# Kernel tuning notes

Hardware: AMD Instinct MI355X
Metric: run time of the kernel (lower is better)

The kernel has to match this reference:

```python
import jax, jax.numpy as jnp
import numpy as np

B, T, L, D = 512, 100, 256, 128
DEPTH = 8                 # perfect binary tree depth -> path length DEPTH+1
P = DEPTH + 1
N_PER_TREE = 2 * L - 1    # 511 nodes per tree (heap layout)
N_TOTAL = T * N_PER_TREE  # 51100 global nodes


def _build_paths():
    # Heap layout per tree: internal nodes 0..L-2, leaves L-1..2L-2.
    # Path for leaf l = chain of heap ancestors from root to leaf.
    local = np.zeros((L, P), dtype=np.int32)
    for l in range(L):
        node = L - 1 + l
        chain = []
        while True:
            chain.append(node)
            if node == 0:
                break
            node = (node - 1) // 2
        local[l] = np.array(chain[::-1], dtype=np.int32)
    offs = (np.arange(T, dtype=np.int32) * N_PER_TREE)[:, None, None]
    return local[None, :, :] + offs  # [T, L, P] global node ids


def setup_inputs() -> dict:
    key = jax.random.key(0)
    k1, k2, k3, k4, k5, k6 = jax.random.split(key, 6)
    paths = jnp.asarray(_build_paths())
    # GBDT multi-hot: exactly one activated leaf per tree per sample
    leaf = jax.random.randint(k1, (B, T), 0, L)
    cross = (jnp.zeros((B, T, L), jnp.float32)
             .at[jnp.arange(B)[:, None], jnp.arange(T)[None, :], leaf]
             .set(1.0)
             .reshape(B, T * L))
    s = 1.0 / float(np.sqrt(D))  # torch LSTM init range
    node_emb = jax.random.normal(k2, (N_TOTAL, D), jnp.float32) * 0.01
    w_ih = jax.random.uniform(k3, (4 * D, D), jnp.float32, -s, s)
    w_hh = jax.random.uniform(k4, (4 * D, D), jnp.float32, -s, s)
    b_ih = jax.random.uniform(k5, (4 * D,), jnp.float32, -s, s)
    b_hh = jax.random.uniform(k6, (4 * D,), jnp.float32, -s, s)
    return {"cross_features": cross, "node_emb": node_emb, "w_ih": w_ih,
            "w_hh": w_hh, "b_ih": b_ih, "b_hh": b_hh, "paths": paths}


def _lstm_last_h(x, w_ih, w_hh, b_ih, b_hh):
    # x: [S, P, D] -> final hidden state [S, D]; torch gate order i, f, g, o
    S = x.shape[0]
    d = w_hh.shape[1]
    bias = b_ih + b_hh

    def step(carry, x_t):
        h, c = carry
        g = x_t @ w_ih.T + h @ w_hh.T + bias          # [S, 4D]
        i, f, gg, o = jnp.split(g, 4, axis=-1)
        c = jax.nn.sigmoid(f) * c + jax.nn.sigmoid(i) * jnp.tanh(gg)
        h = jax.nn.sigmoid(o) * jnp.tanh(c)
        return (h, c), None

    h0 = jnp.zeros((S, d), x.dtype)
    (h, _), _ = jax.lax.scan(step, (h0, h0), jnp.swapaxes(x, 0, 1))
    return h


def reference(cross_features, node_emb, w_ih, w_hh, b_ih, b_hh, paths):
    t, l, p = paths.shape
    b = cross_features.shape[0]
    d = node_emb.shape[1]
    cf = cross_features.reshape(b, t, l)
    leaf = jnp.argmax(cf, axis=-1)                    # [B, T] activated leaf per tree
    active = jnp.any(cf > 0, axis=-1)                 # [B, T] tree has an activated leaf
    node_ids = paths[jnp.arange(t)[None, :], leaf]    # [B, T, P] root-to-leaf global ids
    x = node_emb[node_ids].reshape(b * t, p, d)       # batched path gather
    h = _lstm_last_h(x, w_ih, w_hh, b_ih, b_hh).reshape(b, t, d)
    return jnp.where(active[..., None], h, jnp.zeros((), h.dtype))
```

## Files before the change

### kernel.cpp

```cpp
#include <hip/hip_runtime.h>
#include <math.h>


#define B_N 512
#define T_N 100
#define L_N 256
#define D_N 128
#define NPT 511

typedef __attribute__((ext_vector_type(8))) short short8;
typedef __attribute__((ext_vector_type(4))) float f32x4;
typedef __attribute__((ext_vector_type(4))) unsigned short ushort4v;

__device__ __forceinline__ unsigned short f2bf(float f) {
    unsigned u = __float_as_uint(f);
    return (unsigned short)((u + 0x7FFFu + ((u >> 16) & 1u)) >> 16);
}
__device__ __forceinline__ float bf2f(unsigned short b) {
    return __uint_as_float(((unsigned)b) << 16);
}
__device__ __forceinline__ float fsigmoid(float x) {
    return __builtin_amdgcn_rcpf(1.f + __builtin_amdgcn_exp2f(-1.44269504f * x));
}
__device__ __forceinline__ float ftanh(float x) {
    return 1.f - 2.f * __builtin_amdgcn_rcpf(1.f + __builtin_amdgcn_exp2f(2.88539009f * x));
}
__device__ __forceinline__ void keepreg(short8 &x) {
    asm volatile("" : "+v"(x));
}

__global__ __launch_bounds__(256) void pack_kernel(const float* __restrict__ w_ih,
                                                   const float* __restrict__ w_hh,
                                                   const float* __restrict__ b_ih,
                                                   const float* __restrict__ b_hh,
                                                   unsigned short* __restrict__ Bhi,
                                                   unsigned short* __restrict__ Blo,
                                                   float* __restrict__ bias) {
    const int idx = blockIdx.x * 256 + threadIdx.x;
    const int k  = idx & 255;
    const int np = idx >> 8;
    const float val = (k < 128) ? w_ih[(size_t)np * 128 + k]
                                : w_hh[(size_t)np * 128 + (k - 128)];
    const unsigned short hi = f2bf(val);
    const int kb = k >> 5, krel = k & 31, quad = krel >> 3, e = krel & 7;
    const int tn = np >> 4, col = np & 15, lane = quad * 16 + col;
    Bhi[(((size_t)kb * 32 + tn) * 64 + lane) * 8 + e] = hi;
    if (kb >= 4) {
        const unsigned short lo = f2bf(val - bf2f(hi));
        Blo[((((size_t)kb - 4) * 32 + tn) * 64 + lane) * 8 + e] = lo;
    }
    if (k == 0) bias[np] = b_ih[np] + b_hh[np];
}

__global__ __launch_bounds__(512, 2) void tree_kernel(
    const float* __restrict__ node_emb,
    const unsigned short* __restrict__ Bhi,
    const unsigned short* __restrict__ Blo,
    const float* __restrict__ bias,
    float* __restrict__ h8)
{
    __shared__ float hbuf[2][2][16][132];
    __shared__ float cbuf[2][2][16][132];
    __shared__ float h7buf[2][32][132];
    __shared__ unsigned short AhiF[8 * 4 * 512];
    __shared__ unsigned short AloF[4 * 4 * 512];

    const int tp   = blockIdx.x >> 2;
    const int s    = blockIdx.x & 3;
    const int t0   = tp * 2;
    const int tid  = threadIdx.x;
    const int widx = tid >> 6;
    const int lane = tid & 63;
    const int ml   = lane & 15;
    const int quad = lane >> 4;
    const int j    = widx * 16 + ml;

    const float bi = bias[j];
    const float bf = bias[128 + j];
    const float bg = bias[256 + j];
    const float bo = bias[384 + j];

    const short8* Bh8 = reinterpret_cast<const short8*>(Bhi);
    const short8* Bl8 = reinterpret_cast<const short8*>(Blo);
    const short8* Ah8 = reinterpret_cast<const short8*>(AhiF);
    const short8* Al8 = reinterpret_cast<const short8*>(AloF);

    short8 bhR[8][4], blR[4][4];
    #pragma unroll
    for (int kb = 0; kb < 8; ++kb)
        #pragma unroll
        for (int g = 0; g < 4; ++g)
            bhR[kb][g] = Bh8[(kb * 32 + g * 8 + widx) * 64 + lane];
    #pragma unroll
    for (int kb = 0; kb < 4; ++kb)
        #pragma unroll
        for (int g = 0; g < 4; ++g)
            blR[kb][g] = Bl8[(kb * 32 + g * 8 + widx) * 64 + lane];
    #pragma unroll
    for (int kb = 0; kb < 8; ++kb)
        #pragma unroll
        for (int g = 0; g < 4; ++g)
            keepreg(bhR[kb][g]);
    #pragma unroll
    for (int kb = 0; kb < 4; ++kb)
        #pragma unroll
        for (int g = 0; g < 4; ++g)
            keepreg(blR[kb][g]);

    for (int d = 0; d <= 6; ++d) {
        const int Mrows = (d == 0) ? 1 : (d == 1) ? 2 : (1 << (d - 2));
        const int pbase = (d >= 2) ? (s << (d - 2)) : 0;
        const bool root = (d == 0);
        const int cur = d & 1, prv = cur ^ 1;

        #pragma unroll
        for (int h2 = 0; h2 < 4; ++h2) {
            const int r5 = tid & 31;
            const int u  = r5 >> 4, r = r5 & 15;
            const int k4 = (tid >> 5) + h2 * 16;
            const int k  = k4 * 4;
            int p = r; if (p > Mrows - 1) p = Mrows - 1;
            float4 v;
            if (k < 128) {
                const int local = (1 << d) - 1 + pbase + p;
                v = *reinterpret_cast<const float4*>(
                        node_emb + (size_t)((t0 + u) * NPT + local) * D_N + k);
            } else if (root) {
                v = make_float4(0.f, 0.f, 0.f, 0.f);
            } else {
                const int pr = (d == 2) ? (s >> 1) : (p >> 1);
                v = *reinterpret_cast<const float4*>(&hbuf[prv][u][pr][k - 128]);
            }
            const int kb = k >> 5, qk = (k & 31) >> 3, e0 = k & 4;
            const ushort4v hv = { f2bf(v.x), f2bf(v.y), f2bf(v.z), f2bf(v.w) };
            *reinterpret_cast<ushort4v*>(
                &AhiF[((kb * 4 + u) * 64 + qk * 16 + r) * 8 + e0]) = hv;
            if (k >= 128) {
                const ushort4v lv = { f2bf(v.x - bf2f(hv.x)), f2bf(v.y - bf2f(hv.y)),
                                      f2bf(v.z - bf2f(hv.z)), f2bf(v.w - bf2f(hv.w)) };
                *reinterpret_cast<ushort4v*>(
                    &AloF[(((kb - 4) * 4 + u) * 64 + qk * 16 + r) * 8 + e0]) = lv;
            }
        }
        __syncthreads();

        #pragma unroll
        for (int u = 0; u < 2; ++u) {
            float cpre[4];
            #pragma unroll
            for (int rr = 0; rr < 4; ++rr) {
                int m = quad * 4 + rr;
                if (m > Mrows - 1) m = Mrows - 1;
                const int pr = (d == 2) ? (s >> 1) : (m >> 1);
                cpre[rr] = root ? 0.f : cbuf[prv][u][pr][j];
            }

            f32x4 acc[4];
            #pragma unroll
            for (int g = 0; g < 4; ++g) acc[g] = (f32x4)0.f;

            #pragma unroll
            for (int kb = 0; kb < 8; ++kb) {
                const short8 ah = Ah8[(kb * 4 + u) * 64 + lane];
                short8 al;
                if (kb >= 4) al = Al8[((kb - 4) * 4 + u) * 64 + lane];
                #pragma unroll
                for (int g = 0; g < 4; ++g) {
                    acc[g] = __builtin_amdgcn_mfma_f32_16x16x32_bf16(
                        ah, bhR[kb][g], acc[g], 0, 0, 0);
                    if (kb >= 4) {
                        acc[g] = __builtin_amdgcn_mfma_f32_16x16x32_bf16(
                            ah, blR[kb - 4][g], acc[g], 0, 0, 0);
                        acc[g] = __builtin_amdgcn_mfma_f32_16x16x32_bf16(
                            al, bhR[kb][g], acc[g], 0, 0, 0);
                    }
                }
            }

            #pragma unroll
            for (int rr = 0; rr < 4; ++rr) {
                const int m = quad * 4 + rr;
                if (m < Mrows) {
                    const float ig = fsigmoid(acc[0][rr] + bi);
                    const float fg = fsigmoid(acc[1][rr] + bf);
                    const float gv = ftanh(acc[2][rr] + bg);
                    const float og = fsigmoid(acc[3][rr] + bo);
                    const float cn = fg * cpre[rr] + ig * gv;
                    const float hn = og * ftanh(cn);
                    hbuf[cur][u][m][j] = hn;
                    cbuf[cur][u][m][j] = cn;
                }
            }
        }
        __syncthreads();
    }

    {
        #pragma unroll
        for (int h2 = 0; h2 < 8; ++h2) {
            const int r6 = tid & 63;
            const int u  = r6 >> 5, m = r6 & 31;
            const int k4 = (tid >> 6) + h2 * 8;
            const int k  = k4 * 4;
            const int mt = r6 >> 4, mlr = r6 & 15;
            float4 v;
            if (k < 128) {
                const int local = 127 + s * 32 + m;
                v = *reinterpret_cast<const float4*>(
                        node_emb + (size_t)((t0 + u) * NPT + local) * D_N + k);
            } else {
                v = *reinterpret_cast<const float4*>(&hbuf[0][u][m >> 1][k - 128]);
            }
            const int kb = k >> 5, qk = (k & 31) >> 3, e0 = k & 4;
            const ushort4v hv = { f2bf(v.x), f2bf(v.y), f2bf(v.z), f2bf(v.w) };
            *reinterpret_cast<ushort4v*>(
                &AhiF[((kb * 4 + mt) * 64 + qk * 16 + mlr) * 8 + e0]) = hv;
            if (k >= 128) {
                const ushort4v lv = { f2bf(v.x - bf2f(hv.x)), f2bf(v.y - bf2f(hv.y)),
                                      f2bf(v.z - bf2f(hv.z)), f2bf(v.w - bf2f(hv.w)) };
                *reinterpret_cast<ushort4v*>(
                    &AloF[(((kb - 4) * 4 + mt) * 64 + qk * 16 + mlr) * 8 + e0]) = lv;
            }
        }
        __syncthreads();

        float cpreA[4][4];
        #pragma unroll
        for (int mt = 0; mt < 4; ++mt) {
            const int u = mt >> 1;
            #pragma unroll
            for (int rr = 0; rr < 4; ++rr) {
                const int m = (mt & 1) * 16 + quad * 4 + rr;
                cpreA[mt][rr] = cbuf[0][u][m >> 1][j];
            }
        }
        __syncthreads();

        #pragma unroll
        for (int mt = 0; mt < 4; ++mt) {
            const int u = mt >> 1;
            f32x4 acc[4];
            #pragma unroll
            for (int g = 0; g < 4; ++g) acc[g] = (f32x4)0.f;
            #pragma unroll
            for (int kb = 0; kb < 8; ++kb) {
                const short8 ah = Ah8[(kb * 4 + mt) * 64 + lane];
                short8 al;
                if (kb >= 4) al = Al8[((kb - 4) * 4 + mt) * 64 + lane];
                #pragma unroll
                for (int g = 0; g < 4; ++g) {
                    acc[g] = __builtin_amdgcn_mfma_f32_16x16x32_bf16(
                        ah, bhR[kb][g], acc[g], 0, 0, 0);
                    if (kb >= 4) {
                        acc[g] = __builtin_amdgcn_mfma_f32_16x16x32_bf16(
                            ah, blR[kb - 4][g], acc[g], 0, 0, 0);
                        acc[g] = __builtin_amdgcn_mfma_f32_16x16x32_bf16(
                            al, bhR[kb][g], acc[g], 0, 0, 0);
                    }
                }
            }
            #pragma unroll
            for (int rr = 0; rr < 4; ++rr) {
                const int m = (mt & 1) * 16 + quad * 4 + rr;
                const float ig = fsigmoid(acc[0][rr] + bi);
                const float fg = fsigmoid(acc[1][rr] + bf);
                const float gv = ftanh(acc[2][rr] + bg);
                const float og = fsigmoid(acc[3][rr] + bo);
                const float cn = fg * cpreA[mt][rr] + ig * gv;
                const float hn = og * ftanh(cn);
                h7buf[u][m][j] = hn;
                cbuf[m >> 4][u][m & 15][j] = cn;
            }
        }
        __syncthreads();
    }

    for (int pp = 0; pp < 2; ++pp) {
        #pragma unroll
        for (int h2 = 0; h2 < 8; ++h2) {
            const int r6   = tid & 63;
            const int u    = r6 >> 5, m31 = r6 & 31;
            const int mrow = pp * 32 + m31;
            const int k4   = (tid >> 6) + h2 * 8;
            const int k    = k4 * 4;
            const int mt   = r6 >> 4, mlr = r6 & 15;
            float4 v;
            if (k < 128) {
                const int local = 255 + s * 64 + mrow;
                v = *reinterpret_cast<const float4*>(
                        node_emb + (size_t)((t0 + u) * NPT + local) * D_N + k);
            } else {
                v = *reinterpret_cast<const float4*>(&h7buf[u][mrow >> 1][k - 128]);
            }
            const int kb = k >> 5, qk = (k & 31) >> 3, e0 = k & 4;
            const ushort4v hv = { f2bf(v.x), f2bf(v.y), f2bf(v.z), f2bf(v.w) };
            *reinterpret_cast<ushort4v*>(
                &AhiF[((kb * 4 + mt) * 64 + qk * 16 + mlr) * 8 + e0]) = hv;
            if (k >= 128) {
                const ushort4v lv = { f2bf(v.x - bf2f(hv.x)), f2bf(v.y - bf2f(hv.y)),
                                      f2bf(v.z - bf2f(hv.z)), f2bf(v.w - bf2f(hv.w)) };
                *reinterpret_cast<ushort4v*>(
                    &AloF[(((kb - 4) * 4 + mt) * 64 + qk * 16 + mlr) * 8 + e0]) = lv;
            }
        }
        __syncthreads();

        #pragma unroll
        for (int mt = 0; mt < 4; ++mt) {
            const int u = mt >> 1;
            float cpre[4];
            #pragma unroll
            for (int rr = 0; rr < 4; ++rr) {
                const int mrow = pp * 32 + (mt & 1) * 16 + quad * 4 + rr;
                const int c7r  = mrow >> 1;
                cpre[rr] = cbuf[c7r >> 4][u][c7r & 15][j];
            }
            f32x4 acc[4];
            #pragma unroll
            for (int g = 0; g < 4; ++g) acc[g] = (f32x4)0.f;
            #pragma unroll
            for (int kb = 0; kb < 8; ++kb) {
                const short8 ah = Ah8[(kb * 4 + mt) * 64 + lane];
                short8 al;
                if (kb >= 4) al = Al8[((kb - 4) * 4 + mt) * 64 + lane];
                #pragma unroll
                for (int g = 0; g < 4; ++g) {
                    acc[g] = __builtin_amdgcn_mfma_f32_16x16x32_bf16(
                        ah, bhR[kb][g], acc[g], 0, 0, 0);
                    if (kb >= 4) {
                        acc[g] = __builtin_amdgcn_mfma_f32_16x16x32_bf16(
                            ah, blR[kb - 4][g], acc[g], 0, 0, 0);
                        acc[g] = __builtin_amdgcn_mfma_f32_16x16x32_bf16(
                            al, bhR[kb][g], acc[g], 0, 0, 0);
                    }
                }
            }
            #pragma unroll
            for (int rr = 0; rr < 4; ++rr) {
                const int mrow = pp * 32 + (mt & 1) * 16 + quad * 4 + rr;
                const float ig = fsigmoid(acc[0][rr] + bi);
                const float fg = fsigmoid(acc[1][rr] + bf);
                const float gv = ftanh(acc[2][rr] + bg);
                const float og = fsigmoid(acc[3][rr] + bo);
                const float cn = fg * cpre[rr] + ig * gv;
                const float hn = og * ftanh(cn);
                h8[(size_t)(((t0 + u) << 8) + s * 64 + mrow) * D_N + j] = hn;
            }
        }
        __syncthreads();
    }
}

__global__ __launch_bounds__(256) void gather_kernel(const float* __restrict__ cross,
                                                     const float* __restrict__ h8,
                                                     float* __restrict__ out) {
    const int bt   = blockIdx.x * 4 + (threadIdx.x >> 6);
    const int lane = threadIdx.x & 63;
    const int t    = bt % T_N;
    const float4 v = reinterpret_cast<const float4*>(cross + (size_t)bt * L_N)[lane];
    int idx = -1;
    if      (v.x > 0.f) idx = lane * 4 + 0;
    else if (v.y > 0.f) idx = lane * 4 + 1;
    else if (v.z > 0.f) idx = lane * 4 + 2;
    else if (v.w > 0.f) idx = lane * 4 + 3;
    const unsigned long long m = __ballot(idx >= 0);
    int lf = -1;
    if (m != 0ULL) {
        const int first = __builtin_ctzll(m);
        lf = __shfl(idx, first);
    }
    float2 o = make_float2(0.f, 0.f);
    if (lf >= 0)
        o = reinterpret_cast<const float2*>(h8 + (size_t)(t * L_N + lf) * D_N)[lane];
    reinterpret_cast<float2*>(out + (size_t)bt * D_N)[lane] = o;
}

extern "C" void kernel_launch(void* const* d_in, const int* in_sizes, int n_in,
                              void* d_out, int out_size, void* d_ws, size_t ws_size,
                              hipStream_t stream) {
    const float* cross    = (const float*)d_in[0];
    const float* node_emb = (const float*)d_in[1];
    const float* w_ih     = (const float*)d_in[2];
    const float* w_hh     = (const float*)d_in[3];
    const float* b_ih     = (const float*)d_in[4];
    const float* b_hh     = (const float*)d_in[5];
    float* out = (float*)d_out;
    float* ws  = (float*)d_ws;

    float* h8   = ws;
    float* bias = h8 + (size_t)51200 * D_N;
    unsigned short* Bhi = (unsigned short*)(bias + 512);
    unsigned short* Blo = Bhi + 131072;

    pack_kernel<<<512, 256, 0, stream>>>(w_ih, w_hh, b_ih, b_hh, Bhi, Blo, bias);

    tree_kernel<<<(T_N / 2) * 4, 512, 0, stream>>>(node_emb, Bhi, Blo, bias, h8);

    gather_kernel<<<(B_N * T_N) / 4, 256, 0, stream>>>(cross, h8, out);
}
```

Before: 198.2 us.

## Stream LSTM weights from memory per k-block and reuse across row tiles

```diff
diff --git a/kernel.cpp b/kernel.cpp
--- a/kernel.cpp
+++ b/kernel.cpp
@@ -24,9 +24,6 @@
 }
 __device__ __forceinline__ float ftanh(float x) {
     return 1.f - 2.f * __builtin_amdgcn_rcpf(1.f + __builtin_amdgcn_exp2f(2.88539009f * x));
-}
-__device__ __forceinline__ void keepreg(short8 &x) {
-    asm volatile("" : "+v"(x));
 }
 
 __global__ __launch_bounds__(256) void pack_kernel(const float* __restrict__ w_ih,
@@ -85,28 +82,6 @@
     const short8* Ah8 = reinterpret_cast<const short8*>(AhiF);
     const short8* Al8 = reinterpret_cast<const short8*>(AloF);
 
-    short8 bhR[8][4], blR[4][4];
-    #pragma unroll
-    for (int kb = 0; kb < 8; ++kb)
-        #pragma unroll
-        for (int g = 0; g < 4; ++g)
-            bhR[kb][g] = Bh8[(kb * 32 + g * 8 + widx) * 64 + lane];
-    #pragma unroll
-    for (int kb = 0; kb < 4; ++kb)
-        #pragma unroll
-        for (int g = 0; g < 4; ++g)
-            blR[kb][g] = Bl8[(kb * 32 + g * 8 + widx) * 64 + lane];
-    #pragma unroll
-    for (int kb = 0; kb < 8; ++kb)
-        #pragma unroll
-        for (int g = 0; g < 4; ++g)
-            keepreg(bhR[kb][g]);
-    #pragma unroll
-    for (int kb = 0; kb < 4; ++kb)
-        #pragma unroll
-        for (int g = 0; g < 4; ++g)
-            keepreg(blR[kb][g]);
-
     for (int d = 0; d <= 6; ++d) {
         const int Mrows = (d == 0) ? 1 : (d == 1) ? 2 : (1 << (d - 2));
         const int pbase = (d >= 2) ? (s << (d - 2)) : 0;
@@ -144,48 +119,49 @@
         }
         __syncthreads();
 
+        f32x4 acc[2][4];
+        #pragma unroll
+        for (int u = 0; u < 2; ++u)
+            #pragma unroll
+            for (int g = 0; g < 4; ++g) acc[u][g] = (f32x4)0.f;
+
+        #pragma unroll
+        for (int kb = 0; kb < 8; ++kb) {
+            const short8 ah0 = Ah8[(kb * 4 + 0) * 64 + lane];
+            const short8 ah1 = Ah8[(kb * 4 + 1) * 64 + lane];
+            short8 al0, al1;
+            if (kb >= 4) {
+                al0 = Al8[((kb - 4) * 4 + 0) * 64 + lane];
+                al1 = Al8[((kb - 4) * 4 + 1) * 64 + lane];
+            }
+            #pragma unroll
+            for (int g = 0; g < 4; ++g) {
+                const short8 bh = Bh8[(kb * 32 + g * 8 + widx) * 64 + lane];
+                acc[0][g] = __builtin_amdgcn_mfma_f32_16x16x32_bf16(ah0, bh, acc[0][g], 0, 0, 0);
+                acc[1][g] = __builtin_amdgcn_mfma_f32_16x16x32_bf16(ah1, bh, acc[1][g], 0, 0, 0);
+                if (kb >= 4) {
+                    const short8 bl = Bl8[((kb - 4) * 32 + g * 8 + widx) * 64 + lane];
+                    acc[0][g] = __builtin_amdgcn_mfma_f32_16x16x32_bf16(ah0, bl, acc[0][g], 0, 0, 0);
+                    acc[1][g] = __builtin_amdgcn_mfma_f32_16x16x32_bf16(ah1, bl, acc[1][g], 0, 0, 0);
+                    acc[0][g] = __builtin_amdgcn_mfma_f32_16x16x32_bf16(al0, bh, acc[0][g], 0, 0, 0);
+                    acc[1][g] = __builtin_amdgcn_mfma_f32_16x16x32_bf16(al1, bh, acc[1][g], 0, 0, 0);
+                }
+            }
+        }
+
         #pragma unroll
         for (int u = 0; u < 2; ++u) {
-            float cpre[4];
-            #pragma unroll
-            for (int rr = 0; rr < 4; ++rr) {
-                int m = quad * 4 + rr;
-                if (m > Mrows - 1) m = Mrows - 1;
-                const int pr = (d == 2) ? (s >> 1) : (m >> 1);
-                cpre[rr] = root ? 0.f : cbuf[prv][u][pr][j];
-            }
-
-            f32x4 acc[4];
-            #pragma unroll
-            for (int g = 0; g < 4; ++g) acc[g] = (f32x4)0.f;
-
-            #pragma unroll
-            for (int kb = 0; kb < 8; ++kb) {
-                const short8 ah = Ah8[(kb * 4 + u) * 64 + lane];
-                short8 al;
-                if (kb >= 4) al = Al8[((kb - 4) * 4 + u) * 64 + lane];
-                #pragma unroll
-                for (int g = 0; g < 4; ++g) {
-                    acc[g] = __builtin_amdgcn_mfma_f32_16x16x32_bf16(
-                        ah, bhR[kb][g], acc[g], 0, 0, 0);
-                    if (kb >= 4) {
-                        acc[g] = __builtin_amdgcn_mfma_f32_16x16x32_bf16(
-                            ah, blR[kb - 4][g], acc[g], 0, 0, 0);
-                        acc[g] = __builtin_amdgcn_mfma_f32_16x16x32_bf16(
-                            al, bhR[kb][g], acc[g], 0, 0, 0);
-                    }
-                }
-            }
-
             #pragma unroll
             for (int rr = 0; rr < 4; ++rr) {
                 const int m = quad * 4 + rr;
                 if (m < Mrows) {
-                    const float ig = fsigmoid(acc[0][rr] + bi);
-                    const float fg = fsigmoid(acc[1][rr] + bf);
-                    const float gv = ftanh(acc[2][rr] + bg);
-                    const float og = fsigmoid(acc[3][rr] + bo);
-                    const float cn = fg * cpre[rr] + ig * gv;
+                    const int pr = (d == 2) ? (s >> 1) : (m >> 1);
+                    const float cp = root ? 0.f : cbuf[prv][u][pr][j];
+                    const float ig = fsigmoid(acc[u][0][rr] + bi);
+                    const float fg = fsigmoid(acc[u][1][rr] + bf);
+                    const float gv = ftanh(acc[u][2][rr] + bg);
+                    const float og = fsigmoid(acc[u][3][rr] + bo);
+                    const float cn = fg * cp + ig * gv;
                     const float hn = og * ftanh(cn);
                     hbuf[cur][u][m][j] = hn;
                     cbuf[cur][u][m][j] = cn;
@@ -224,52 +200,53 @@
         }
         __syncthreads();
 
-        float cpreA[4][4];
+        f32x4 acc[4][4];
+        #pragma unroll
+        for (int mt = 0; mt < 4; ++mt)
+            #pragma unroll
+            for (int g = 0; g < 4; ++g) acc[mt][g] = (f32x4)0.f;
+
+        #pragma unroll
+        for (int kb = 0; kb < 8; ++kb) {
+            short8 ah[4], al[4];
+            #pragma unroll
+            for (int mt = 0; mt < 4; ++mt) {
+                ah[mt] = Ah8[(kb * 4 + mt) * 64 + lane];
+                if (kb >= 4) al[mt] = Al8[((kb - 4) * 4 + mt) * 64 + lane];
+            }
+            #pragma unroll
+            for (int g = 0; g < 4; ++g) {
+                const short8 bh = Bh8[(kb * 32 + g * 8 + widx) * 64 + lane];
+                #pragma unroll
+                for (int mt = 0; mt < 4; ++mt)
+                    acc[mt][g] = __builtin_amdgcn_mfma_f32_16x16x32_bf16(ah[mt], bh, acc[mt][g], 0, 0, 0);
+                if (kb >= 4) {
+                    const short8 bl = Bl8[((kb - 4) * 32 + g * 8 + widx) * 64 + lane];
+                    #pragma unroll
+                    for (int mt = 0; mt < 4; ++mt) {
+                        acc[mt][g] = __builtin_amdgcn_mfma_f32_16x16x32_bf16(ah[mt], bl, acc[mt][g], 0, 0, 0);
+                        acc[mt][g] = __builtin_amdgcn_mfma_f32_16x16x32_bf16(al[mt], bh, acc[mt][g], 0, 0, 0);
+                    }
+                }
+            }
+        }
+
         #pragma unroll
         for (int mt = 0; mt < 4; ++mt) {
             const int u = mt >> 1;
             #pragma unroll
             for (int rr = 0; rr < 4; ++rr) {
                 const int m = (mt & 1) * 16 + quad * 4 + rr;
-                cpreA[mt][rr] = cbuf[0][u][m >> 1][j];
-            }
-        }
-        __syncthreads();
-
-        #pragma unroll
-        for (int mt = 0; mt < 4; ++mt) {
-            const int u = mt >> 1;
-            f32x4 acc[4];
-            #pragma unroll
-            for (int g = 0; g < 4; ++g) acc[g] = (f32x4)0.f;
-            #pragma unroll
-            for (int kb = 0; kb < 8; ++kb) {
-                const short8 ah = Ah8[(kb * 4 + mt) * 64 + lane];
-                short8 al;
-                if (kb >= 4) al = Al8[((kb - 4) * 4 + mt) * 64 + lane];
-                #pragma unroll
-                for (int g = 0; g < 4; ++g) {
-                    acc[g] = __builtin_amdgcn_mfma_f32_16x16x32_bf16(
-                        ah, bhR[kb][g], acc[g], 0, 0, 0);
-                    if (kb >= 4) {
-                        acc[g] = __builtin_amdgcn_mfma_f32_16x16x32_bf16(
-                            ah, blR[kb - 4][g], acc[g], 0, 0, 0);
-                        acc[g] = __builtin_amdgcn_mfma_f32_16x16x32_bf16(
-                            al, bhR[kb][g], acc[g], 0, 0, 0);
-                    }
-                }
-            }
-            #pragma unroll
-            for (int rr = 0; rr < 4; ++rr) {
-                const int m = (mt & 1) * 16 + quad * 4 + rr;
-                const float ig = fsigmoid(acc[0][rr] + bi);
-                const float fg = fsigmoid(acc[1][rr] + bf);
-                const float gv = ftanh(acc[2][rr] + bg);
-                const float og = fsigmoid(acc[3][rr] + bo);
-                const float cn = fg * cpreA[mt][rr] + ig * gv;
+                const float cp = cbuf[0][u][m >> 1][j];
+                const float ig = fsigmoid(acc[mt][0][rr] + bi);
+                const float fg = fsigmoid(acc[mt][1][rr] + bf);
+                const float gv = ftanh(acc[mt][2][rr] + bg);
+                const float og = fsigmoid(acc[mt][3][rr] + bo);
+                const float cn = fg * cp + ig * gv;
                 const float hn = og * ftanh(cn);
                 h7buf[u][m][j] = hn;
-                cbuf[m >> 4][u][m & 15][j] = cn;
+                if (m < 16) cbuf[1][u][m][j] = cn;
+                else        hbuf[1][u][m - 16][j] = cn;
             }
         }
         __syncthreads();
@@ -305,44 +282,51 @@
         }
         __syncthreads();
 
+        f32x4 acc[4][4];
+        #pragma unroll
+        for (int mt = 0; mt < 4; ++mt)
+            #pragma unroll
+            for (int g = 0; g < 4; ++g) acc[mt][g] = (f32x4)0.f;
+
+        #pragma unroll
+        for (int kb = 0; kb < 8; ++kb) {
+            short8 ah[4], al[4];
+            #pragma unroll
+            for (int mt = 0; mt < 4; ++mt) {
+                ah[mt] = Ah8[(kb * 4 + mt) * 64 + lane];
+                if (kb >= 4) al[mt] = Al8[((kb - 4) * 4 + mt) * 64 + lane];
+            }
+            #pragma unroll
+            for (int g = 0; g < 4; ++g) {
+                const short8 bh = Bh8[(kb * 32 + g * 8 + widx) * 64 + lane];
+                #pragma unroll
+                for (int mt = 0; mt < 4; ++mt)
+                    acc[mt][g] = __builtin_amdgcn_mfma_f32_16x16x32_bf16(ah[mt], bh, acc[mt][g], 0, 0, 0);
+                if (kb >= 4) {
+                    const short8 bl = Bl8[((kb - 4) * 32 + g * 8 + widx) * 64 + lane];
+                    #pragma unroll
+                    for (int mt = 0; mt < 4; ++mt) {
+                        acc[mt][g] = __builtin_amdgcn_mfma_f32_16x16x32_bf16(ah[mt], bl, acc[mt][g], 0, 0, 0);
+                        acc[mt][g] = __builtin_amdgcn_mfma_f32_16x16x32_bf16(al[mt], bh, acc[mt][g], 0, 0, 0);
+                    }
+                }
+            }
+        }
+
         #pragma unroll
         for (int mt = 0; mt < 4; ++mt) {
             const int u = mt >> 1;
-            float cpre[4];
             #pragma unroll
             for (int rr = 0; rr < 4; ++rr) {
                 const int mrow = pp * 32 + (mt & 1) * 16 + quad * 4 + rr;
                 const int c7r  = mrow >> 1;
-                cpre[rr] = cbuf[c7r >> 4][u][c7r & 15][j];
-            }
-            f32x4 acc[4];
-            #pragma unroll
-            for (int g = 0; g < 4; ++g) acc[g] = (f32x4)0.f;
-            #pragma unroll
-            for (int kb = 0; kb < 8; ++kb) {
-                const short8 ah = Ah8[(kb * 4 + mt) * 64 + lane];
-                short8 al;
-                if (kb >= 4) al = Al8[((kb - 4) * 4 + mt) * 64 + lane];
-                #pragma unroll
-                for (int g = 0; g < 4; ++g) {
-                    acc[g] = __builtin_amdgcn_mfma_f32_16x16x32_bf16(
-                        ah, bhR[kb][g], acc[g], 0, 0, 0);
-                    if (kb >= 4) {
-                        acc[g] = __builtin_amdgcn_mfma_f32_16x16x32_bf16(
-                            ah, blR[kb - 4][g], acc[g], 0, 0, 0);
-                        acc[g] = __builtin_amdgcn_mfma_f32_16x16x32_bf16(
-                            al, bhR[kb][g], acc[g], 0, 0, 0);
-                    }
-                }
-            }
-            #pragma unroll
-            for (int rr = 0; rr < 4; ++rr) {
-                const int mrow = pp * 32 + (mt & 1) * 16 + quad * 4 + rr;
-                const float ig = fsigmoid(acc[0][rr] + bi);
-                const float fg = fsigmoid(acc[1][rr] + bf);
-                const float gv = ftanh(acc[2][rr] + bg);
-                const float og = fsigmoid(acc[3][rr] + bo);
-                const float cn = fg * cpre[rr] + ig * gv;
+                const float cp = (pp == 0) ? cbuf[1][u][c7r][j]
+                                           : hbuf[1][u][c7r - 16][j];
+                const float ig = fsigmoid(acc[mt][0][rr] + bi);
+                const float fg = fsigmoid(acc[mt][1][rr] + bf);
+                const float gv = ftanh(acc[mt][2][rr] + bg);
+                const float og = fsigmoid(acc[mt][3][rr] + bo);
+                const float cn = fg * cp + ig * gv;
                 const float hn = og * ftanh(cn);
                 h8[(size_t)(((t0 + u) << 8) + s * 64 + mrow) * D_N + j] = hn;
             }
```

New measurement: 242.4 us. 22.3% more time.
